# Kernel optimization log

Measured on AMD Instinct MI355X. Metric: run time of the kernel, lower is better.

Reference implementation:

```python
import jax, jax.numpy as jnp
import numpy as np

ALPHA = 2000.0   # alpha (bandwidth penalty)
K = 8            # number of modes
MAX_N = 20       # max ADMM iterations; tol=0 -> loop always runs MAX_N-1 iters
DC = False


def setup_inputs() -> dict:
    key = jax.random.key(0)
    signal = jax.random.normal(key, (16, 8192), dtype=jnp.float32)  # (C, T)
    return {"signal": signal}


def _forward(signal):
    C, T = signal.shape
    F = 2 * T
    # mirror extension -> (C, 2T)
    f = jnp.concatenate([signal[:, :T // 2][:, ::-1], signal, signal[:, T // 2:][:, ::-1]], axis=1)
    t = jnp.linspace(1.0 / F, 1.0, F)
    freqs = (t - 0.5 - 1.0 / F).astype(jnp.float32)                  # (F,)
    # NOTE: torch.fft.fftshift with default dim shifts ALL dims (incl. channel dim);
    # jnp.fft.fftshift with axes=None matches this behavior exactly.
    f_hat = jnp.fft.fftshift(jnp.fft.fft(f))
    f_hat_plus = f_hat.at[:, :F // 2].set(0)                         # zero negative freqs
    fpos = f_hat_plus.T.astype(jnp.complex64)                        # (F, C)
    freqs_c = freqs.astype(jnp.complex64)
    fh = freqs[F // 2:]                                              # positive freqs (F/2,)
    alpha_c = jnp.complex64(ALPHA)

    omega0 = ((0.5 / K) * jnp.arange(K, dtype=jnp.float32)).astype(jnp.complex64)  # init == 1
    u0 = jnp.zeros((F, K, C), jnp.complex64)
    sum0 = jnp.zeros((F, C), jnp.complex64)

    def omega_update(u_k):                                           # u_k: (F, C)
        p = jnp.abs(u_k[F // 2:, :]) ** 2                            # (F/2, C)
        return (jnp.sum(fh @ p) / jnp.sum(p)).astype(jnp.complex64)

    def step(carry, _):
        u_prev, omega_prev, sum_uk = carry
        sum_uk = sum_uk + u_prev[:, K - 1, :] - u_prev[:, 0, :]
        us, omegas = [], []
        for k in range(K):                                           # sequential mode recurrence
            if k > 0:
                sum_uk = sum_uk + us[k - 1] - u_prev[:, k, :]
            # torch uses omega from the PREVIOUS outer iteration for all modes
            denom = 1.0 + alpha_c * jnp.square(freqs_c - omega_prev[k])   # (F,)
            u_k = (fpos - sum_uk) / denom[:, None]   # lamda_hat stays 0 (never updated in torch)
            us.append(u_k)
            if k == 0 and DC:
                omegas.append(jnp.complex64(0.0))
            else:
                omegas.append(omega_update(u_k))
        u_curr = jnp.stack(us, axis=1)                               # (F, K, C)
        omega_curr = jnp.stack(omegas)                               # (K,)
        return (u_curr, omega_curr, sum_uk), omega_curr

    (u_fin, _, _), omega_hist = jax.lax.scan(step, (u0, omega0, sum0), None, length=MAX_N - 1)
    omega = jnp.concatenate([omega0[None, :], omega_hist], axis=0)   # (MAX_N, K)

    # Hermitian completion of the half-spectrum (matches torch index assignments & order)
    pos = u_fin[F // 2:, :, :]                                       # (F/2, K, C)
    u_hat = jnp.zeros((F, K, C), jnp.complex64)
    u_hat = u_hat.at[F // 2:].set(pos)
    u_hat = u_hat.at[jnp.arange(F // 2, 0, -1)].set(jnp.conj(pos))   # overwrites bin F/2 w/ conj
    u_hat = u_hat.at[0].set(jnp.conj(u_hat[-1]))

    u_time = jnp.fft.ifft(jnp.fft.ifftshift(u_hat, axes=0), axis=0).real  # (F, K, C)
    u_c = jnp.transpose(u_time, (1, 0, 2)).astype(jnp.complex64)          # (K, F, C)
    u_c = u_c[:, F // 4:3 * F // 4, :]                                    # crop mirror -> (K, T, C)
    u_hat2 = jnp.conj(jnp.fft.fftshift(jnp.fft.fft(u_c, axis=1), axes=1)) # (K, T, C)
    u_hat2 = jnp.transpose(u_hat2, (1, 0, 2))                             # (T, K, C)
    # torch applies ifftshift with dim=-1, which is the CHANNEL dim here; replicate faithfully
    u_out = jnp.fft.ifftshift(u_c, axes=-1).real                          # (K, T, C)
    return u_out, u_hat2, omega


def reference(signal):
    return _forward(signal)
```

## Files before the change

### kernel.cpp

```cpp
#include <hip/hip_runtime.h>
#include <math.h>

#define NPAIR 131072
#define STEPS 19
#define VMD_BLOCKS 256

#define SW(a) ((a) ^ (((a) >> 5) & 31))

#define LD_RLX(p)    __hip_atomic_load((p),       __ATOMIC_RELAXED, __HIP_MEMORY_SCOPE_AGENT)
#define ST_RLX(p,v)  __hip_atomic_store((p),(v),  __ATOMIC_RELAXED, __HIP_MEMORY_SCOPE_AGENT)
#define FAA_RLX(p,v) __hip_atomic_fetch_add((p),(v),__ATOMIC_RELAXED, __HIP_MEMORY_SCOPE_AGENT)

#define D_P     0
#define D_CNT   77824
#define D_OHIST 78368
#define D_TOTAL 78512

__device__ __forceinline__ float2 cadd(float2 a, float2 b){ return make_float2(a.x+b.x, a.y+b.y); }
__device__ __forceinline__ float2 csub(float2 a, float2 b){ return make_float2(a.x-b.x, a.y-b.y); }
__device__ __forceinline__ float2 cmul(float2 a, float2 b){
    return make_float2(a.x*b.x - a.y*b.y, a.x*b.y + a.y*b.x);
}
template<int SGN>
__device__ __forceinline__ float2 imul(float2 a){
    return (SGN > 0) ? make_float2(-a.y, a.x) : make_float2(a.y, -a.x);
}

template<int SGN>
__device__ __forceinline__ void dft8(const float2* a, float2* y){
    const float C = 0.70710678118654752f;
    const float sg = (SGN > 0) ? 1.f : -1.f;
    float2 t0 = cadd(a[0], a[4]), t1 = csub(a[0], a[4]);
    float2 t2 = cadd(a[2], a[6]), t3 = imul<SGN>(csub(a[2], a[6]));
    float2 E0 = cadd(t0, t2), E2 = csub(t0, t2), E1 = cadd(t1, t3), E3 = csub(t1, t3);
    float2 s0 = cadd(a[1], a[5]), s1 = csub(a[1], a[5]);
    float2 s2 = cadd(a[3], a[7]), s3 = imul<SGN>(csub(a[3], a[7]));
    float2 O0 = cadd(s0, s2), O2 = csub(s0, s2), O1 = cadd(s1, s3), O3 = csub(s1, s3);
    float2 w1 = make_float2(C, sg * C), w3 = make_float2(-C, sg * C);
    float2 R0 = O0, R1 = cmul(O1, w1), R2 = imul<SGN>(O2), R3 = cmul(O3, w3);
    y[0] = cadd(E0, R0); y[4] = csub(E0, R0);
    y[1] = cadd(E1, R1); y[5] = csub(E1, R1);
    y[2] = cadd(E2, R2); y[6] = csub(E2, R2);
    y[3] = cadd(E3, R3); y[7] = csub(E3, R3);
}

template<int SGN>
__device__ void lds_fft8192_r8(float2* lds, int tid){
    #pragma unroll
    for (int pi = 0; pi < 4; pi++){
        int ls = 3 * pi;
        int s  = 1 << ls;
        int nn = 8192 >> ls;
        int q = tid & (s - 1);
        float2 a[8], y[8];
        #pragma unroll
        for (int r = 0; r < 8; r++) a[r] = lds[SW(tid + (r << 10))];
        __syncthreads();
        dft8<SGN>(a, y);
        int p = tid >> ls;
        float ang = (float)(2 * p) / (float)nn;
        float sn, cs;
        sincospif(SGN > 0 ? ang : -ang, &sn, &cs);
        float2 w = make_float2(cs, sn);
        float2 wk = make_float2(1.f, 0.f);
        int o = q + ((tid - q) << 3);
        lds[SW(o)] = y[0];
        #pragma unroll
        for (int k = 1; k < 8; k++){
            wk = cmul(wk, w);
            lds[SW(o + (k << ls))] = cmul(y[k], wk);
        }
        __syncthreads();
    }
    #pragma unroll
    for (int w4 = 0; w4 < 4; w4++){
        int idx = (w4 << 10) + tid;
        float2 a = lds[SW(idx)], b = lds[SW(idx + 4096)];
        lds[SW(idx)]        = cadd(a, b);
        lds[SW(idx + 4096)] = csub(a, b);
    }
    __syncthreads();
}

template<int SGN>
__device__ void lds_fft4096_r8(float2* lds, int tid){
    #pragma unroll
    for (int pi = 0; pi < 4; pi++){
        int ls = 3 * pi;
        int s  = 1 << ls;
        int nn = 4096 >> ls;
        float2 a[8], y[8];
        int q = tid & (s - 1);
        if (tid < 512){
            #pragma unroll
            for (int r = 0; r < 8; r++) a[r] = lds[SW(tid + (r << 9))];
        }
        __syncthreads();
        if (tid < 512){
            dft8<SGN>(a, y);
            int p = tid >> ls;
            float ang = (float)(2 * p) / (float)nn;
            float sn, cs;
            sincospif(SGN > 0 ? ang : -ang, &sn, &cs);
            float2 w = make_float2(cs, sn);
            float2 wk = make_float2(1.f, 0.f);
            int o = q + ((tid - q) << 3);
            lds[SW(o)] = y[0];
            #pragma unroll
            for (int k = 1; k < 8; k++){
                wk = cmul(wk, w);
                lds[SW(o + (k << ls))] = cmul(y[k], wk);
            }
        }
        __syncthreads();
    }
}

__global__ __launch_bounds__(1024) void k_stageA(const float* __restrict__ sig,
                                                 float2* __restrict__ FPTA,
                                                 float2* __restrict__ FPTB,
                                                 double* __restrict__ D){
    extern __shared__ float2 lds[];
    int tid  = threadIdx.x;
    int bb   = blockIdx.x;
    int zi = bb * 1024 + tid;
    if (zi < 544) D[D_CNT + zi] = 0.0;
    int cw   = bb >> 1, half = bb & 1;
    int cs   = (cw + 8) & 15;
    const float* sp = sig + cs * 8192;
    #pragma unroll
    for (int r = 0; r < 8; r++){
        int p = r * 1024 + tid;
        int x = 2 * p + half;
        int mx = (x < 4096) ? (4095 - x) : ((x < 12288) ? (x - 4096) : (20479 - x));
        lds[SW(p)] = make_float2(sp[mx], 0.f);
    }
    __syncthreads();
    lds_fft8192_r8<-1>(lds, tid);
    float2* dst = (half == 0 ? FPTA : FPTB) + cw * 8192;
    #pragma unroll
    for (int r = 0; r < 8; r++){
        int j = r * 1024 + tid;
        dst[j] = lds[SW(j)];
    }
}

__global__ __launch_bounds__(512, 2) void k_vmd_all(const float2* __restrict__ FPTA,
                                                    const float2* __restrict__ FPTB,
                                                    float2* __restrict__ U,
                                                    double* __restrict__ D){
    double* P     = D + D_P;
    int*    CNT   = (int*)(D + D_CNT);
    double* OHIST = D + D_OHIST;

    int tid = blockIdx.x * 512 + threadIdx.x;
    int j = tid & 8191;
    double fr = (double)j / 16384.0;
    float2 Av = FPTA[tid], Bv = FPTB[tid];
    float snw, cnw;
    sincospif(-(float)j / 8192.0f, &snw, &cnw);
    float2 tw = cmul(Bv, make_float2(cnw, snw));
    float2 fv = make_float2(Av.x + tw.x, Av.y + tw.y);
    double fx = fv.x, fy = fv.y;
    float urx[8], ury[8];
    double om[8];
    #pragma unroll
    for (int k = 0; k < 8; k++){ urx[k] = 0.f; ury[k] = 0.f; om[k] = 0.0625 * (double)k; }
    __shared__ double lred[8][16];
    __shared__ double ndls[256];
    __shared__ double om_s[8];
    int lane = threadIdx.x & 63, wv = threadIdx.x >> 6;
    int grp = blockIdx.x >> 4;

    for (int step = 0; step < STEPS; step++){
        if (step > 0){
            #pragma unroll
            for (int k = 0; k < 8; k++) om[k] = om_s[k];
        }
        double sx = 0.0, sy = 0.0;
        #pragma unroll
        for (int k = 1; k < 8; k++){ sx += (double)urx[k]; sy += (double)ury[k]; }
        double lx = 0.0, ly = 0.0, nloc[8], dloc[8];
        #pragma unroll
        for (int k = 0; k < 8; k++){
            if (k > 0){ sx += lx - (double)urx[k]; sy += ly - (double)ury[k]; }
            double d = fr - om[k];
            double den = 1.0 + 2000.0 * d * d;
            double rden = 1.0 / den;
            double nx = (fx - sx) * rden, ny = (fy - sy) * rden;
            urx[k] = (float)nx; ury[k] = (float)ny;
            lx = nx; ly = ny;
            double pw = nx * nx + ny * ny;
            nloc[k] = fr * pw; dloc[k] = pw;
        }
        double s8[8];
        {
            bool hi = (lane & 32) != 0;
            #pragma unroll
            for (int k = 0; k < 8; k++){
                double t = hi ? nloc[k] : dloc[k];
                double r = __shfl_xor(t, 32);
                s8[k] = (hi ? dloc[k] : nloc[k]) + r;
            }
        }
        double s4v[4];
        {
            bool hi = (lane & 16) != 0;
            #pragma unroll
            for (int k = 0; k < 4; k++){
                double t = hi ? s8[k] : s8[k + 4];
                double r = __shfl_xor(t, 16);
                s4v[k] = (hi ? s8[k + 4] : s8[k]) + r;
            }
        }
        double s2v[2];
        {
            bool hi = (lane & 8) != 0;
            #pragma unroll
            for (int k = 0; k < 2; k++){
                double t = hi ? s4v[k] : s4v[k + 2];
                double r = __shfl_xor(t, 8);
                s2v[k] = (hi ? s4v[k + 2] : s4v[k]) + r;
            }
        }
        double sv;
        {
            bool hi = (lane & 4) != 0;
            double t = hi ? s2v[0] : s2v[1];
            double r = __shfl_xor(t, 4);
            sv = (hi ? s2v[1] : s2v[0]) + r;
        }
        sv += __shfl_xor(sv, 2);
        sv += __shfl_xor(sv, 1);
        if ((lane & 3) == 0) lred[wv][lane >> 2] = sv;
        __syncthreads();
        if (threadIdx.x < 16){
            double sum = 0.0;
            #pragma unroll
            for (int w = 0; w < 8; w++) sum += lred[w][threadIdx.x];
            ST_RLX(&P[step * 4096 + blockIdx.x * 16 + threadIdx.x], sum);
        }
        __syncthreads();
        if (step < STEPS - 1){
            if (threadIdx.x == 0){
                int target = 16 * (step + 1);
                int old = FAA_RLX(&CNT[grp * 32], 1);
                bool released = false;
                if (old == target - 1){
                    int rold = FAA_RLX(&CNT[512], 1);
                    if (rold == target - 1){
                        #pragma unroll
                        for (int g = 0; g < 16; g++)
                            ST_RLX(&CNT[576 + g * 32], step + 1);
                        released = true;
                    }
                }
                if (!released)
                    while (LD_RLX(&CNT[576 + grp * 32]) <= step)
                        __builtin_amdgcn_s_sleep(1);
            }
            __syncthreads();
            if (threadIdx.x < 256){
                int slot = threadIdx.x & 15, rg = threadIdx.x >> 4;
                const double* q = &P[step * 4096 + rg * 256 + slot];
                double s = 0.0;
                #pragma unroll
                for (int i = 0; i < 16; i++) s += LD_RLX(&q[i * 16]);
                ndls[rg * 16 + slot] = s;
            }
            __syncthreads();
            if (threadIdx.x < 8){
                double n_ = 0.0, d_ = 0.0;
                #pragma unroll
                for (int bk = 0; bk < 16; bk++){
                    n_ += ndls[bk * 16 + threadIdx.x];
                    d_ += ndls[bk * 16 + 8 + threadIdx.x];
                }
                double v = n_ / d_;
                om_s[threadIdx.x] = v;
                if (blockIdx.x == 0)
                    ST_RLX(&OHIST[step * 8 + threadIdx.x], v);
            }
            __syncthreads();
        }
    }
    #pragma unroll
    for (int k = 0; k < 8; k++) U[k * NPAIR + tid] = make_float2(urx[k], ury[k]);
}

__global__ __launch_bounds__(1024) void k_stageCD(float2* __restrict__ U){
    extern __shared__ float2 lds[];
    int tid = threadIdx.x;
    int b = blockIdx.x;
    const float2* pos = U + b * 8192;
    float* slice = (float*)(U) + (size_t)b * 16384;
    const float inv = 1.0f / 16384.0f;
    #pragma unroll
    for (int r = 0; r < 8; r++){
        int p = r * 1024 + tid;
        float2 Hk, HkM;
        if (p == 0){
            Hk  = make_float2(pos[0].x, 0.f);
            HkM = make_float2(pos[8191].x, 0.f);
        } else {
            Hk = pos[p];
            float2 q2 = pos[8192 - p];
            HkM = make_float2(q2.x, -q2.y);
        }
        float2 S  = cadd(Hk, HkM);
        float2 Dv = csub(Hk, HkM);
        float sn, cn;
        sincospif((float)p / 8192.0f, &sn, &cn);
        float2 c = cmul(make_float2(cn, sn), Dv);
        lds[SW(p)] = make_float2(S.x - c.y, S.y + c.x);
    }
    __syncthreads();
    lds_fft8192_r8<1>(lds, tid);
    float2 zreg[4];
    #pragma unroll
    for (int q = 2; q < 6; q++){
        int n = q * 1024 + tid;
        float2 z = lds[SW(n)];
        zreg[q - 2] = make_float2(z.x * inv, z.y * inv);
        *(float2*)&slice[2 * n - 4096] = zreg[q - 2];
    }
    __syncthreads();
    #pragma unroll
    for (int q = 0; q < 4; q++)
        lds[SW(q * 1024 + tid)] = zreg[q];
    __syncthreads();
    lds_fft4096_r8<-1>(lds, tid);
    #pragma unroll
    for (int q = 0; q < 4; q++){
        int k = q * 1024 + tid;
        float2 Wk = lds[SW(k)];
        float2 Wm = lds[SW((4096 - k) & 4095)];
        float ax = 0.5f * (Wk.x + Wm.x);
        float dx = Wk.x - Wm.x, dy = Wk.y + Wm.y;
        float bx = 0.5f * dy, by = -0.5f * dx;
        float sn, cn;
        sincospif(-(float)k / 4096.0f, &sn, &cn);
        float rey = ax + cn * bx - sn * by;
        slice[12288 + k] = rey;
        if (k > 0) slice[12288 - k] = rey;
        else       slice[8192]      = Wk.x - Wk.y;
    }
}

__global__ __launch_bounds__(256) void k_outs(const float* __restrict__ U32,
                                              const double* __restrict__ Dbase,
                                              float* __restrict__ out){
    __shared__ double smemd[128 * 65 / 2 + 140];
    float* smem = (float*)smemd;
    int bx = blockIdx.x;
    int tid = threadIdx.x;
    if (bx < 256){
        float (*tile)[257] = (float(*)[257])smem;
        int k  = bx >> 5;
        int t0 = (bx & 31) * 256;
        #pragma unroll
        for (int cw = 0; cw < 16; cw++)
            tile[cw][tid] = U32[((size_t)(k * 16 + cw)) * 16384 + t0 + tid];
        __syncthreads();
        #pragma unroll
        for (int i = 0; i < 16; i++){
            int flat = i * 256 + tid;
            int dt = flat >> 4, ch = flat & 15;
            int cw = (ch + 8) & 15;
            out[(size_t)k * 131072 + t0 * 16 + flat] = tile[cw][dt];
        }
    } else if (bx < 384){
        float (*tile)[65] = (float(*)[65])smem;
        int t0 = (bx - 256) * 64;
        #pragma unroll
        for (int i = 0; i < 32; i++){
            int flat = i * 256 + tid;
            int b = flat >> 6, dt = flat & 63;
            tile[b][dt] = U32[(size_t)b * 16384 + 8192 + t0 + dt];
        }
        __syncthreads();
        #pragma unroll
        for (int i = 0; i < 32; i++){
            int flat = i * 256 + tid;
            int dt = flat >> 7, b = flat & 127;
            out[1048576 + (size_t)(t0 + dt) * 128 + b] = tile[b][dt];
        }
    } else {
        const double* P     = Dbase + D_P;
        const double* OHIST = Dbase + D_OHIST;
        double* dsm = smemd;
        if (tid < 256){
            int slot = tid & 15, rg = tid >> 4;
            const double* q = &P[18 * 4096 + rg * 256 + slot];
            double s = 0.0;
            #pragma unroll
            for (int i = 0; i < 16; i++) s += q[i * 16];
            dsm[tid] = s;
        }
        __syncthreads();
        if (tid < 8){
            double n_ = 0.0, d_ = 0.0;
            #pragma unroll
            for (int bk = 0; bk < 16; bk++){
                n_ += dsm[bk * 16 + tid];
                d_ += dsm[bk * 16 + 8 + tid];
            }
            dsm[256 + tid] = n_ / d_;
        }
        __syncthreads();
        if (tid < 160){
            int row = tid >> 3, k = tid & 7;
            double v;
            if (row == 0)       v = 0.0625 * (double)k;
            else if (row <= 18) v = OHIST[(row - 1) * 8 + k];
            else                v = dsm[256 + k];
            out[2097152 + tid] = (float)v;
        }
    }
}

extern "C" void kernel_launch(void* const* d_in, const int* in_sizes, int n_in,
                              void* d_out, int out_size, void* d_ws, size_t ws_size,
                              hipStream_t stream){
    const float* sig = (const float*)d_in[0];
    float* out = (float*)d_out;
    char* p = (char*)d_ws;
    float2* U    = (float2*)p;
    float2* FPTA = (float2*)p;
    float2* FPTB = (float2*)(p + (size_t)1 * 1024 * 1024);
    double* D    = (double*)(p + (size_t)8 * 1024 * 1024);

    k_stageA<<<dim3(32), dim3(1024), 65536, stream>>>(sig, FPTA, FPTB, D);
    k_vmd_all<<<dim3(VMD_BLOCKS), dim3(512), 0, stream>>>(FPTA, FPTB, U, D);
    k_stageCD<<<dim3(128), dim3(1024), 65536, stream>>>(U);
    k_outs<<<dim3(385), dim3(256), 0, stream>>>((const float*)U, D, out);
}
```

Baseline: 173.4 us.

## Split stage-A FFT into four sub-FFTs and bank-reduce omega partials atomically

Stage A now computes four 4096-point FFTs per channel over 64 blocks of 512 threads, instead of two 8192-point FFTs over 32 blocks. The VMD kernel merges them with a radix-4 twiddle combine, which gives the front end more parallel blocks. The per-step omega partial sums are now accumulated with double atomicAdd into 16 banks, replacing per-block slots. After each grid barrier every block reads one value per thread instead of summing 16 strided loads, which shortens the critical path of the barrier. The cost is atomic contention and a nondeterministic summation order in fp64.

```diff
diff --git a/kernel.cpp b/kernel.cpp
--- a/kernel.cpp
+++ b/kernel.cpp
@@ -4,6 +4,7 @@
 #define NPAIR 131072
 #define STEPS 19
 #define VMD_BLOCKS 256
+#define ND_BANKS 16
 
 #define SW(a) ((a) ^ (((a) >> 5) & 31))
 
@@ -11,10 +12,9 @@
 #define ST_RLX(p,v)  __hip_atomic_store((p),(v),  __ATOMIC_RELAXED, __HIP_MEMORY_SCOPE_AGENT)
 #define FAA_RLX(p,v) __hip_atomic_fetch_add((p),(v),__ATOMIC_RELAXED, __HIP_MEMORY_SCOPE_AGENT)
 
-#define D_P     0
-#define D_CNT   77824
-#define D_OHIST 78368
-#define D_TOTAL 78512
+#define D_NDB   0
+#define D_CNT   4864
+#define D_OHIST 5400
 
 __device__ __forceinline__ float2 cadd(float2 a, float2 b){ return make_float2(a.x+b.x, a.y+b.y); }
 __device__ __forceinline__ float2 csub(float2 a, float2 b){ return make_float2(a.x-b.x, a.y-b.y); }
@@ -116,51 +116,55 @@
     }
 }
 
-__global__ __launch_bounds__(1024) void k_stageA(const float* __restrict__ sig,
-                                                 float2* __restrict__ FPTA,
-                                                 float2* __restrict__ FPTB,
-                                                 double* __restrict__ D){
+__global__ __launch_bounds__(512) void k_stageA(const float* __restrict__ sig,
+                                                float2* __restrict__ C,
+                                                double* __restrict__ D){
     extern __shared__ float2 lds[];
-    int tid  = threadIdx.x;
-    int bb   = blockIdx.x;
-    int zi = bb * 1024 + tid;
-    if (zi < 544) D[D_CNT + zi] = 0.0;
-    int cw   = bb >> 1, half = bb & 1;
-    int cs   = (cw + 8) & 15;
+    int tid = threadIdx.x;
+    int bb  = blockIdx.x;
+    int zi = bb * 512 + tid;
+    if (zi < 5400) D[zi] = 0.0;
+    int cw = bb >> 2, r4 = bb & 3;
+    int cs = (cw + 8) & 15;
     const float* sp = sig + cs * 8192;
     #pragma unroll
-    for (int r = 0; r < 8; r++){
-        int p = r * 1024 + tid;
-        int x = 2 * p + half;
+    for (int i = 0; i < 8; i++){
+        int p = i * 512 + tid;
+        int x = 4 * p + r4;
         int mx = (x < 4096) ? (4095 - x) : ((x < 12288) ? (x - 4096) : (20479 - x));
         lds[SW(p)] = make_float2(sp[mx], 0.f);
     }
     __syncthreads();
-    lds_fft8192_r8<-1>(lds, tid);
-    float2* dst = (half == 0 ? FPTA : FPTB) + cw * 8192;
-    #pragma unroll
-    for (int r = 0; r < 8; r++){
-        int j = r * 1024 + tid;
+    lds_fft4096_r8<-1>(lds, tid);
+    float2* dst = C + (size_t)bb * 4096;
+    #pragma unroll
+    for (int i = 0; i < 8; i++){
+        int j = i * 512 + tid;
         dst[j] = lds[SW(j)];
     }
 }
 
-__global__ __launch_bounds__(512, 2) void k_vmd_all(const float2* __restrict__ FPTA,
-                                                    const float2* __restrict__ FPTB,
+__global__ __launch_bounds__(512, 2) void k_vmd_all(const float2* __restrict__ C,
                                                     float2* __restrict__ U,
                                                     double* __restrict__ D){
-    double* P     = D + D_P;
+    double* NDB   = D + D_NDB;
     int*    CNT   = (int*)(D + D_CNT);
     double* OHIST = D + D_OHIST;
 
     int tid = blockIdx.x * 512 + threadIdx.x;
     int j = tid & 8191;
+    int cw = tid >> 13;
     double fr = (double)j / 16384.0;
-    float2 Av = FPTA[tid], Bv = FPTB[tid];
-    float snw, cnw;
-    sincospif(-(float)j / 8192.0f, &snw, &cnw);
-    float2 tw = cmul(Bv, make_float2(cnw, snw));
-    float2 fv = make_float2(Av.x + tw.x, Av.y + tw.y);
+    {
+    }
+    const float2* Cb = C + (size_t)(cw * 4) * 4096;
+    int m = j & 4095;
+    float2 C0 = Cb[m], C1 = Cb[4096 + m], C2 = Cb[8192 + m], C3 = Cb[12288 + m];
+    float s1, c1, s2, c2;
+    sincospif(-(float)j / 8192.0f, &s1, &c1);
+    sincospif(-(float)j / 4096.0f, &s2, &c2);
+    float2 w1 = make_float2(c1, s1), w2 = make_float2(c2, s2), w3 = cmul(w1, w2);
+    float2 fv = cadd(cadd(C0, cmul(w1, C1)), cadd(cmul(w2, C2), cmul(w3, C3)));
     double fx = fv.x, fy = fv.y;
     float urx[8], ury[8];
     double om[8];
@@ -170,6 +174,7 @@
     __shared__ double ndls[256];
     __shared__ double om_s[8];
     int lane = threadIdx.x & 63, wv = threadIdx.x >> 6;
+    int mybank = (blockIdx.x & (ND_BANKS - 1)) * 16;
     int grp = blockIdx.x >> 4;
 
     for (int step = 0; step < STEPS; step++){
@@ -238,7 +243,7 @@
             double sum = 0.0;
             #pragma unroll
             for (int w = 0; w < 8; w++) sum += lred[w][threadIdx.x];
-            ST_RLX(&P[step * 4096 + blockIdx.x * 16 + threadIdx.x], sum);
+            atomicAdd(&NDB[step * 256 + mybank + threadIdx.x], sum);
         }
         __syncthreads();
         if (step < STEPS - 1){
@@ -260,19 +265,13 @@
                         __builtin_amdgcn_s_sleep(1);
             }
             __syncthreads();
-            if (threadIdx.x < 256){
-                int slot = threadIdx.x & 15, rg = threadIdx.x >> 4;
-                const double* q = &P[step * 4096 + rg * 256 + slot];
-                double s = 0.0;
-                #pragma unroll
-                for (int i = 0; i < 16; i++) s += LD_RLX(&q[i * 16]);
-                ndls[rg * 16 + slot] = s;
-            }
+            if (threadIdx.x < 256)
+                ndls[threadIdx.x] = LD_RLX(&NDB[step * 256 + threadIdx.x]);
             __syncthreads();
             if (threadIdx.x < 8){
                 double n_ = 0.0, d_ = 0.0;
                 #pragma unroll
-                for (int bk = 0; bk < 16; bk++){
+                for (int bk = 0; bk < ND_BANKS; bk++){
                     n_ += ndls[bk * 16 + threadIdx.x];
                     d_ += ndls[bk * 16 + 8 + threadIdx.x];
                 }
@@ -386,22 +385,15 @@
             out[1048576 + (size_t)(t0 + dt) * 128 + b] = tile[b][dt];
         }
     } else {
-        const double* P     = Dbase + D_P;
+        const double* NDB   = Dbase + D_NDB;
         const double* OHIST = Dbase + D_OHIST;
         double* dsm = smemd;
-        if (tid < 256){
-            int slot = tid & 15, rg = tid >> 4;
-            const double* q = &P[18 * 4096 + rg * 256 + slot];
-            double s = 0.0;
-            #pragma unroll
-            for (int i = 0; i < 16; i++) s += q[i * 16];
-            dsm[tid] = s;
-        }
+        if (tid < 256) dsm[tid] = NDB[18 * 256 + tid];
         __syncthreads();
         if (tid < 8){
             double n_ = 0.0, d_ = 0.0;
             #pragma unroll
-            for (int bk = 0; bk < 16; bk++){
+            for (int bk = 0; bk < ND_BANKS; bk++){
                 n_ += dsm[bk * 16 + tid];
                 d_ += dsm[bk * 16 + 8 + tid];
             }
@@ -425,13 +417,12 @@
     const float* sig = (const float*)d_in[0];
     float* out = (float*)d_out;
     char* p = (char*)d_ws;
-    float2* U    = (float2*)p;
-    float2* FPTA = (float2*)p;
-    float2* FPTB = (float2*)(p + (size_t)1 * 1024 * 1024);
-    double* D    = (double*)(p + (size_t)8 * 1024 * 1024);
-
-    k_stageA<<<dim3(32), dim3(1024), 65536, stream>>>(sig, FPTA, FPTB, D);
-    k_vmd_all<<<dim3(VMD_BLOCKS), dim3(512), 0, stream>>>(FPTA, FPTB, U, D);
+    float2* U = (float2*)p;
+    float2* C = (float2*)p;
+    double* D = (double*)(p + (size_t)8 * 1024 * 1024);
+
+    k_stageA<<<dim3(64), dim3(512), 32768, stream>>>(sig, C, D);
+    k_vmd_all<<<dim3(VMD_BLOCKS), dim3(512), 0, stream>>>(C, U, D);
     k_stageCD<<<dim3(128), dim3(1024), 65536, stream>>>(U);
     k_outs<<<dim3(385), dim3(256), 0, stream>>>((const float*)U, D, out);
 }
```

Measured after the change: 161.3 us. 7.0% less time.
